# Performance work log

Measured on AMD Instinct MI355X. Metric: run time of the kernel, lower is better.

## Reference

```python
import jax, jax.numpy as jnp
import numpy as np

VOCAB = 50257
EMBED = 256
UNITS = 1024   # dec_units == attention units == GRU units
ENC_D = 1024   # encoder feature dim
B = 64
T_ENC = 128


def setup_inputs() -> dict:
    key = jax.random.key(0)
    ks = jax.random.split(key, 16)
    s = lambda k, *sh: jax.random.normal(k, sh, dtype=jnp.float32) * 0.02
    gru_in = ENC_D + EMBED  # concat(context, embedding)
    return {
        "x": jax.random.randint(ks[0], (B, 1), 0, VOCAB),
        "hidden": jax.random.normal(ks[1], (B, UNITS), dtype=jnp.float32),
        "enc_output": jax.random.normal(ks[2], (B, T_ENC, ENC_D), dtype=jnp.float32),
        "emb": s(ks[3], VOCAB, EMBED),
        "W1": s(ks[4], UNITS, UNITS), "b1": jnp.zeros((UNITS,), jnp.float32),
        "W2": s(ks[5], ENC_D, UNITS), "b2": jnp.zeros((UNITS,), jnp.float32),
        "V": s(ks[6], UNITS, 1), "bV": jnp.zeros((1,), jnp.float32),
        "gru_kernel": s(ks[7], gru_in, 3 * UNITS),
        "gru_rkernel": s(ks[8], UNITS, 3 * UNITS),
        "gru_bias": jnp.zeros((2, 3 * UNITS), jnp.float32),  # reset_after=True: [input_bias, recurrent_bias]
        "fcW": s(ks[9], UNITS, VOCAB), "fcb": jnp.zeros((VOCAB,), jnp.float32),
    }


def reference(x, hidden, enc_output, emb, W1, b1, W2, b2, V, bV,
              gru_kernel, gru_rkernel, gru_bias, fcW, fcb):
    # --- Bahdanau attention ---
    q = hidden[:, None, :] @ W1 + b1                    # [B,1,U]
    k = enc_output @ W2 + b2                            # [B,T,U]
    score = jnp.tanh(q + k) @ V + bV                    # [B,T,1]
    attw = jax.nn.softmax(score, axis=1)                # [B,T,1]
    context = jnp.sum(attw * enc_output, axis=1)        # [B,ENC_D]

    # --- embed token and concat (single time step) ---
    e = emb[x[:, 0]]                                    # [B,EMBED]
    xin = jnp.concatenate([context, e], axis=-1)        # [B,ENC_D+EMBED]

    # --- single GRU step (keras default reset_after=True), initial state zeros
    # (original code calls self.gru(x) without initial_state) ---
    h0 = jnp.zeros((xin.shape[0], UNITS), xin.dtype)
    xz, xr, xh = jnp.split(xin @ gru_kernel + gru_bias[0], 3, axis=-1)
    rz, rr, rh = jnp.split(h0 @ gru_rkernel + gru_bias[1], 3, axis=-1)
    z = jax.nn.sigmoid(xz + rz)
    r = jax.nn.sigmoid(xr + rr)
    hh = jnp.tanh(xh + r * rh)
    h = z * h0 + (1.0 - z) * hh                          # [B,U]

    logits = h @ fcW + fcb                               # [B,VOCAB]
    return logits, h, attw
```

## Files before the change

kernel.cpp:

```cpp
#include <hip/hip_runtime.h>
#include <hip/hip_bf16.h>

#define UNITS 1024
#define EMBED 256
#define TENC  128
#define BATCH 64
#define VOCAB 50257
#define GRU_IN 1280
#define MROWS 8192
#define NCB   8

typedef __bf16 bf16x8 __attribute__((ext_vector_type(8)));
typedef __bf16 bf16x2 __attribute__((ext_vector_type(2)));
typedef float  f32x4  __attribute__((ext_vector_type(4)));
typedef float  f32x4u __attribute__((ext_vector_type(4), aligned(4)));

__global__ __launch_bounds__(256) void gemm_splitk(
    const float* __restrict__ A, const float* __restrict__ B,
    float* __restrict__ Cpart, int M, int N, int K, int Kc)
{
  const int row0  = blockIdx.x * 64;
  const int col0  = blockIdx.y * 64;
  const int kbase = blockIdx.z * Kc;
  const int tid  = threadIdx.x;
  const int lane = tid & 63;
  const int wid  = tid >> 6;
  const int wm   = (wid >> 1) * 32;
  const int wn   = (wid & 1) * 32;

  __shared__ __bf16 As[4][64][8];
  __shared__ __bf16 Bs[4][64][8];

  f32x4 acc[2][2] = {};

  const int ar  = tid >> 2;
  const int akc = (tid & 3) * 8;
  const int bkk = tid >> 4;
  const int bn  = (tid & 15) * 4;

  f32x4 pa0 = {}, pa1 = {}, pb0 = {}, pb1 = {};

  auto LOAD = [&](int k0) {
    if (row0 + ar < M) {
      const float* ap = A + (size_t)(row0 + ar) * K + k0 + akc;
      pa0 = *reinterpret_cast<const f32x4*>(ap);
      pa1 = *reinterpret_cast<const f32x4*>(ap + 4);
    }
    const float* bp0 = B + (size_t)(k0 + bkk) * N + col0 + bn;
    pb0 = *reinterpret_cast<const f32x4*>(bp0);
    pb1 = *reinterpret_cast<const f32x4*>(bp0 + (size_t)16 * N);
  };

  LOAD(kbase);
  const int nt = Kc >> 5;
  for (int t = 0; t < nt; ++t) {
    __syncthreads();
    {
      bf16x8 v;
#pragma unroll
      for (int j = 0; j < 4; ++j) { v[j] = (__bf16)pa0[j]; v[4 + j] = (__bf16)pa1[j]; }
      *reinterpret_cast<bf16x8*>(&As[tid & 3][ar][0]) = v;
#pragma unroll
      for (int j = 0; j < 4; ++j) {
        Bs[bkk >> 3][bn + j][bkk & 7]               = (__bf16)pb0[j];
        Bs[(bkk + 16) >> 3][bn + j][(bkk + 16) & 7] = (__bf16)pb1[j];
      }
    }
    __syncthreads();
    if (t + 1 < nt) LOAD(kbase + ((t + 1) << 5));

    bf16x8 af[2], bfr[2];
#pragma unroll
    for (int f = 0; f < 2; ++f) {
      af[f]  = *reinterpret_cast<const bf16x8*>(&As[lane >> 4][wm + f * 16 + (lane & 15)][0]);
      bfr[f] = *reinterpret_cast<const bf16x8*>(&Bs[lane >> 4][wn + f * 16 + (lane & 15)][0]);
    }
#pragma unroll
    for (int fm = 0; fm < 2; ++fm)
#pragma unroll
      for (int fn = 0; fn < 2; ++fn)
        acc[fm][fn] = __builtin_amdgcn_mfma_f32_16x16x32_bf16(af[fm], bfr[fn], acc[fm][fn], 0, 0, 0);
  }

  float* Cz = Cpart + (size_t)blockIdx.z * M * N;
#pragma unroll
  for (int fm = 0; fm < 2; ++fm) {
    const int rbase = row0 + wm + fm * 16 + (lane >> 4) * 4;
#pragma unroll
    for (int fn = 0; fn < 2; ++fn) {
      const int gc = col0 + wn + fn * 16 + (lane & 15);
#pragma unroll
      for (int r = 0; r < 4; ++r) {
        const int gr = rbase + r;
        if (gr < M) Cz[(size_t)gr * N + gc] = acc[fm][fn][r];
      }
    }
  }
}

__global__ __launch_bounds__(256) void gemm_fc(
    const float* __restrict__ A, const float* __restrict__ B,
    const float* __restrict__ bias, float* __restrict__ C, int N)
{
  const int col0 = blockIdx.x * 64;
  const int tid  = threadIdx.x;
  const int lane = tid & 63;
  const int wid  = tid >> 6;
  const int wm   = (wid >> 1) * 32;
  const int wn   = (wid & 1) * 32;

  __shared__ __bf16 As[4][64][8];
  __shared__ __bf16 Bs[4][64][8];

  f32x4 acc[2][2] = {};

  const int ar  = tid >> 2;
  const int akc = (tid & 3) * 8;
  const int bkk = tid >> 4;
  const int bn  = (tid & 15) * 4;

  f32x4 pa0, pa1, pb0, pb1;

  auto LOAD = [&](int k0) {
    const float* ap = A + (size_t)ar * UNITS + k0 + akc;
    pa0 = *reinterpret_cast<const f32x4*>(ap);
    pa1 = *reinterpret_cast<const f32x4*>(ap + 4);
    const int gn = col0 + bn;
    const float* bp0 = B + (size_t)(k0 + bkk) * N + gn;
    const float* bp1 = bp0 + (size_t)16 * N;
    if (gn + 3 < N) {
      pb0 = __builtin_nontemporal_load(reinterpret_cast<const f32x4u*>(bp0));
      pb1 = __builtin_nontemporal_load(reinterpret_cast<const f32x4u*>(bp1));
    } else {
      pb0 = (f32x4){0,0,0,0}; pb1 = (f32x4){0,0,0,0};
#pragma unroll
      for (int j = 0; j < 4; ++j)
        if (gn + j < N) { pb0[j] = bp0[j]; pb1[j] = bp1[j]; }
    }
  };

  LOAD(0);
  for (int t = 0; t < 32; ++t) {
    __syncthreads();
    {
      bf16x8 v;
#pragma unroll
      for (int j = 0; j < 4; ++j) { v[j] = (__bf16)pa0[j]; v[4 + j] = (__bf16)pa1[j]; }
      *reinterpret_cast<bf16x8*>(&As[tid & 3][ar][0]) = v;
#pragma unroll
      for (int j = 0; j < 4; ++j) {
        Bs[bkk >> 3][bn + j][bkk & 7]               = (__bf16)pb0[j];
        Bs[(bkk + 16) >> 3][bn + j][(bkk + 16) & 7] = (__bf16)pb1[j];
      }
    }
    __syncthreads();
    if (t + 1 < 32) LOAD((t + 1) << 5);

    bf16x8 af[2], bfr[2];
#pragma unroll
    for (int f = 0; f < 2; ++f) {
      af[f]  = *reinterpret_cast<const bf16x8*>(&As[lane >> 4][wm + f * 16 + (lane & 15)][0]);
      bfr[f] = *reinterpret_cast<const bf16x8*>(&Bs[lane >> 4][wn + f * 16 + (lane & 15)][0]);
    }
#pragma unroll
    for (int fm = 0; fm < 2; ++fm)
#pragma unroll
      for (int fn = 0; fn < 2; ++fn)
        acc[fm][fn] = __builtin_amdgcn_mfma_f32_16x16x32_bf16(af[fm], bfr[fn], acc[fm][fn], 0, 0, 0);
  }

#pragma unroll
  for (int fm = 0; fm < 2; ++fm) {
    const int rbase = wm + fm * 16 + (lane >> 4) * 4;
#pragma unroll
    for (int fn = 0; fn < 2; ++fn) {
      const int gc = col0 + wn + fn * 16 + (lane & 15);
      if (gc >= N) continue;
      const float bv = bias[gc];
#pragma unroll
      for (int r = 0; r < 4; ++r)
        __builtin_nontemporal_store(acc[fm][fn][r] + bv, &C[(size_t)(rbase + r) * N + gc]);
    }
  }
}

__global__ __launch_bounds__(256) void gemm_k_score(
    const float* __restrict__ enc, const float* __restrict__ W2,
    const float* __restrict__ b1, const float* __restrict__ b2,
    const float* __restrict__ qpart, const float* __restrict__ Vw,
    float* __restrict__ partial)
{
  const int b    = blockIdx.x;
  const int row0 = b * TENC;
  const int col0 = blockIdx.y * 128;
  const int tid  = threadIdx.x;
  const int lane = tid & 63;
  const int wid  = tid >> 6;
  const int wm   = (wid >> 1) * 64;
  const int wn   = (wid & 1) * 64;

  __shared__ __bf16 As[4][128][8];
  __shared__ __bf16 Bs[4][128][8];
  __shared__ float  sred[2][128];

  f32x4 acc[4][4] = {};

  const int ar  = tid >> 1;
  const int ak  = (tid & 1) * 16;
  const int kkp = (tid >> 4) * 2;
  const int c0  = (tid & 15) * 8;

  f32x4 pa[4], pb[4];

  auto LOAD = [&](int k0) {
    const float* ap = enc + (size_t)(row0 + ar) * UNITS + k0 + ak;
    pa[0] = *reinterpret_cast<const f32x4*>(ap);
    pa[1] = *reinterpret_cast<const f32x4*>(ap + 4);
    pa[2] = *reinterpret_cast<const f32x4*>(ap + 8);
    pa[3] = *reinterpret_cast<const f32x4*>(ap + 12);
    const float* bp0 = W2 + (size_t)(k0 + kkp) * UNITS + col0 + c0;
    pb[0] = *reinterpret_cast<const f32x4*>(bp0);
    pb[1] = *reinterpret_cast<const f32x4*>(bp0 + 4);
    pb[2] = *reinterpret_cast<const f32x4*>(bp0 + UNITS);
    pb[3] = *reinterpret_cast<const f32x4*>(bp0 + UNITS + 4);
  };

  LOAD(0);
  for (int t = 0; t < 32; ++t) {
    __syncthreads();
    {
      bf16x8 v0, v1;
#pragma unroll
      for (int j = 0; j < 4; ++j) {
        v0[j] = (__bf16)pa[0][j]; v0[4 + j] = (__bf16)pa[1][j];
        v1[j] = (__bf16)pa[2][j]; v1[4 + j] = (__bf16)pa[3][j];
      }
      *reinterpret_cast<bf16x8*>(&As[(ak >> 3) + 0][ar][0]) = v0;
      *reinterpret_cast<bf16x8*>(&As[(ak >> 3) + 1][ar][0]) = v1;
      const int bch = kkp >> 3, bk = kkp & 7;
#pragma unroll
      for (int j = 0; j < 8; ++j) {
        const float lo = (j < 4) ? pb[0][j] : pb[1][j - 4];
        const float hi = (j < 4) ? pb[2][j] : pb[3][j - 4];
        bf16x2 pr = { (__bf16)lo, (__bf16)hi };
        *reinterpret_cast<bf16x2*>(&Bs[bch][c0 + j][bk]) = pr;
      }
    }
    __syncthreads();
    if (t + 1 < 32) LOAD((t + 1) << 5);

    bf16x8 af[4], bfr[4];
#pragma unroll
    for (int f = 0; f < 4; ++f) {
      af[f]  = *reinterpret_cast<const bf16x8*>(&As[lane >> 4][wm + f * 16 + (lane & 15)][0]);
      bfr[f] = *reinterpret_cast<const bf16x8*>(&Bs[lane >> 4][wn + f * 16 + (lane & 15)][0]);
    }
#pragma unroll
    for (int fm = 0; fm < 4; ++fm)
#pragma unroll
      for (int fn = 0; fn < 4; ++fn)
        acc[fm][fn] = __builtin_amdgcn_mfma_f32_16x16x32_bf16(af[fm], bfr[fn], acc[fm][fn], 0, 0, 0);
  }

  float rowsum[4][4] = {};
#pragma unroll
  for (int fn = 0; fn < 4; ++fn) {
    const int gc = col0 + wn + fn * 16 + (lane & 15);
    float qv = b1[gc] + b2[gc];
#pragma unroll
    for (int s = 0; s < 4; ++s) qv += qpart[(size_t)s * BATCH * UNITS + (size_t)b * UNITS + gc];
    const float vv = Vw[gc];
#pragma unroll
    for (int fm = 0; fm < 4; ++fm)
#pragma unroll
      for (int r = 0; r < 4; ++r)
        rowsum[fm][r] += tanhf(qv + acc[fm][fn][r]) * vv;
  }
#pragma unroll
  for (int off = 8; off; off >>= 1)
#pragma unroll
    for (int fm = 0; fm < 4; ++fm)
#pragma unroll
      for (int r = 0; r < 4; ++r)
        rowsum[fm][r] += __shfl_xor(rowsum[fm][r], off);
  if ((lane & 15) == 0) {
#pragma unroll
    for (int fm = 0; fm < 4; ++fm)
#pragma unroll
      for (int r = 0; r < 4; ++r)
        sred[wid & 1][wm + fm * 16 + (lane >> 4) * 4 + r] = rowsum[fm][r];
  }
  __syncthreads();
  if (tid < TENC)
    partial[(size_t)blockIdx.y * MROWS + row0 + tid] = sred[0][tid] + sred[1][tid];
}

__global__ __launch_bounds__(256) void ctx_kernel(
    const float* __restrict__ enc, const float* __restrict__ partial,
    const float* __restrict__ bV, const float* __restrict__ emb,
    const int* __restrict__ x, float* __restrict__ attw,
    float* __restrict__ xin)
{
  const int b   = blockIdx.x;
  const int tid = threadIdx.x;
  __shared__ float scs[TENC];
  __shared__ float red[4];

  if (tid < TENC) {
    float s = bV[0];
#pragma unroll
    for (int cb = 0; cb < NCB; ++cb) s += partial[(size_t)cb * MROWS + b * TENC + tid];
    float m = s;
#pragma unroll
    for (int off = 32; off; off >>= 1) m = fmaxf(m, __shfl_xor(m, off));
    if ((tid & 63) == 0) red[tid >> 6] = m;
    scs[tid] = s;
  }
  __syncthreads();
  const float mm = fmaxf(red[0], red[1]);
  if (tid < TENC) {
    const float e = expf(scs[tid] - mm);
    scs[tid] = e;
    float su = e;
#pragma unroll
    for (int off = 32; off; off >>= 1) su += __shfl_xor(su, off);
    if ((tid & 63) == 0) red[2 + (tid >> 6)] = su;
  }
  __syncthreads();
  const float inv = 1.f / (red[2] + red[3]);
  if (tid < TENC) scs[tid] *= inv;
  __syncthreads();

  if (blockIdx.y == 0 && tid < TENC) attw[(size_t)b * TENC + tid] = scs[tid];

  const int n = blockIdx.y * 256 + tid;
  const float* ep = enc + (size_t)b * TENC * UNITS + n;
  float c = 0.f;
#pragma unroll 8
  for (int t = 0; t < TENC; ++t) c += scs[t] * ep[(size_t)t * UNITS];
  xin[(size_t)b * GRU_IN + n] = c;
  if (blockIdx.y == 0)
    xin[(size_t)b * GRU_IN + UNITS + tid] = emb[(size_t)x[b] * EMBED + tid];
}

__global__ __launch_bounds__(256) void gru_pw(
    const float* __restrict__ gpart, const float* __restrict__ gb0,
    const float* __restrict__ gb1, float* __restrict__ h)
{
  const int i = blockIdx.x * 256 + threadIdx.x;
  const int b = i >> 10, n = i & 1023;
  float xz = gb0[n], xr = gb0[1024 + n], xh = gb0[2048 + n];
#pragma unroll
  for (int s = 0; s < 4; ++s) {
    const float* g = gpart + (size_t)s * BATCH * 3072 + (size_t)b * 3072;
    xz += g[n]; xr += g[1024 + n]; xh += g[2048 + n];
  }
  const float rz = gb1[n], rr = gb1[1024 + n], rh = gb1[2048 + n];
  const float z = 1.f / (1.f + expf(-(xz + rz)));
  const float r = 1.f / (1.f + expf(-(xr + rr)));
  const float hh = tanhf(xh + r * rh);
  h[i] = (1.f - z) * hh;
}

extern "C" void kernel_launch(void* const* d_in, const int* in_sizes, int n_in,
                              void* d_out, int out_size, void* d_ws, size_t ws_size,
                              hipStream_t stream)
{
  (void)in_sizes; (void)n_in; (void)out_size; (void)ws_size;
  const int*   x      = (const int*)  d_in[0];
  const float* hidden = (const float*)d_in[1];
  const float* enc    = (const float*)d_in[2];
  const float* emb    = (const float*)d_in[3];
  const float* W1     = (const float*)d_in[4];
  const float* b1     = (const float*)d_in[5];
  const float* W2     = (const float*)d_in[6];
  const float* b2     = (const float*)d_in[7];
  const float* Vw     = (const float*)d_in[8];
  const float* bV     = (const float*)d_in[9];
  const float* gk     = (const float*)d_in[10];
  const float* gb     = (const float*)d_in[12];
  const float* fcW    = (const float*)d_in[13];
  const float* fcb    = (const float*)d_in[14];

  float* ws      = (float*)d_ws;
  float* qpart   = ws;
  float* partial = qpart + 262144;
  float* xin     = partial + 65536;
  float* gpart   = xin + 81920;

  float* out    = (float*)d_out;
  float* logits = out;
  float* hout   = out + (size_t)BATCH * VOCAB;
  float* attw   = hout + BATCH * UNITS;

  hipLaunchKernelGGL(gemm_splitk, dim3(1, 16, 4), dim3(256), 0, stream,
                     hidden, W1, qpart, 64, 1024, 1024, 256);
  hipLaunchKernelGGL(gemm_k_score, dim3(64, NCB), dim3(256), 0, stream,
                     enc, W2, b1, b2, qpart, Vw, partial);
  hipLaunchKernelGGL(ctx_kernel, dim3(64, 4), dim3(256), 0, stream,
                     enc, partial, bV, emb, x, attw, xin);
  hipLaunchKernelGGL(gemm_splitk, dim3(1, 48, 4), dim3(256), 0, stream,
                     xin, gk, gpart, 64, 3072, 1280, 320);
  hipLaunchKernelGGL(gru_pw, dim3(256), dim3(256), 0, stream,
                     gpart, gb, gb + 3072, hout);
  hipLaunchKernelGGL(gemm_fc, dim3((VOCAB + 63) / 64), dim3(256), 0, stream,
                     hout, fcW, fcb, logits, VOCAB);
}
```

Measured before the change: 162.7 us.

## Double-buffer LDS in split-K and FC GEMMs, double split-K factor

```diff
diff --git a/kernel.cpp b/kernel.cpp
--- a/kernel.cpp
+++ b/kernel.cpp
@@ -9,6 +9,7 @@
 #define GRU_IN 1280
 #define MROWS 8192
 #define NCB   8
+#define NSPLIT 8
 
 typedef __bf16 bf16x8 __attribute__((ext_vector_type(8)));
 typedef __bf16 bf16x2 __attribute__((ext_vector_type(2)));
@@ -19,7 +20,6 @@
     const float* __restrict__ A, const float* __restrict__ B,
     float* __restrict__ Cpart, int M, int N, int K, int Kc)
 {
-  const int row0  = blockIdx.x * 64;
   const int col0  = blockIdx.y * 64;
   const int kbase = blockIdx.z * Kc;
   const int tid  = threadIdx.x;
@@ -28,8 +28,8 @@
   const int wm   = (wid >> 1) * 32;
   const int wn   = (wid & 1) * 32;
 
-  __shared__ __bf16 As[4][64][8];
-  __shared__ __bf16 Bs[4][64][8];
+  __shared__ __bf16 As[2][4][64][8];
+  __shared__ __bf16 Bs[2][4][64][8];
 
   f32x4 acc[2][2] = {};
 
@@ -38,62 +38,69 @@
   const int bkk = tid >> 4;
   const int bn  = (tid & 15) * 4;
 
-  f32x4 pa0 = {}, pa1 = {}, pb0 = {}, pb1 = {};
-
-  auto LOAD = [&](int k0) {
-    if (row0 + ar < M) {
-      const float* ap = A + (size_t)(row0 + ar) * K + k0 + akc;
-      pa0 = *reinterpret_cast<const f32x4*>(ap);
-      pa1 = *reinterpret_cast<const f32x4*>(ap + 4);
-    }
+  f32x4 pa0[2], pa1[2], pb0[2], pb1[2];
+
+  auto LOAD = [&](int k0, int s) {
+    const float* ap = A + (size_t)ar * K + k0 + akc;
+    pa0[s] = *reinterpret_cast<const f32x4*>(ap);
+    pa1[s] = *reinterpret_cast<const f32x4*>(ap + 4);
     const float* bp0 = B + (size_t)(k0 + bkk) * N + col0 + bn;
-    pb0 = *reinterpret_cast<const f32x4*>(bp0);
-    pb1 = *reinterpret_cast<const f32x4*>(bp0 + (size_t)16 * N);
-  };
-
-  LOAD(kbase);
-  const int nt = Kc >> 5;
-  for (int t = 0; t < nt; ++t) {
-    __syncthreads();
-    {
-      bf16x8 v;
-#pragma unroll
-      for (int j = 0; j < 4; ++j) { v[j] = (__bf16)pa0[j]; v[4 + j] = (__bf16)pa1[j]; }
-      *reinterpret_cast<bf16x8*>(&As[tid & 3][ar][0]) = v;
-#pragma unroll
-      for (int j = 0; j < 4; ++j) {
-        Bs[bkk >> 3][bn + j][bkk & 7]               = (__bf16)pb0[j];
-        Bs[(bkk + 16) >> 3][bn + j][(bkk + 16) & 7] = (__bf16)pb1[j];
-      }
-    }
-    __syncthreads();
-    if (t + 1 < nt) LOAD(kbase + ((t + 1) << 5));
-
+    pb0[s] = *reinterpret_cast<const f32x4*>(bp0);
+    pb1[s] = *reinterpret_cast<const f32x4*>(bp0 + (size_t)16 * N);
+  };
+  auto STAGE = [&](int s, int bb) {
+    bf16x8 v;
+#pragma unroll
+    for (int j = 0; j < 4; ++j) { v[j] = (__bf16)pa0[s][j]; v[4 + j] = (__bf16)pa1[s][j]; }
+    *reinterpret_cast<bf16x8*>(&As[bb][tid & 3][ar][0]) = v;
+#pragma unroll
+    for (int j = 0; j < 4; ++j) {
+      Bs[bb][bkk >> 3][bn + j][bkk & 7]               = (__bf16)pb0[s][j];
+      Bs[bb][(bkk + 16) >> 3][bn + j][(bkk + 16) & 7] = (__bf16)pb1[s][j];
+    }
+  };
+  auto COMPUTE = [&](int bb) {
     bf16x8 af[2], bfr[2];
 #pragma unroll
     for (int f = 0; f < 2; ++f) {
-      af[f]  = *reinterpret_cast<const bf16x8*>(&As[lane >> 4][wm + f * 16 + (lane & 15)][0]);
-      bfr[f] = *reinterpret_cast<const bf16x8*>(&Bs[lane >> 4][wn + f * 16 + (lane & 15)][0]);
+      af[f]  = *reinterpret_cast<const bf16x8*>(&As[bb][lane >> 4][wm + f * 16 + (lane & 15)][0]);
+      bfr[f] = *reinterpret_cast<const bf16x8*>(&Bs[bb][lane >> 4][wn + f * 16 + (lane & 15)][0]);
     }
 #pragma unroll
     for (int fm = 0; fm < 2; ++fm)
 #pragma unroll
       for (int fn = 0; fn < 2; ++fn)
         acc[fm][fn] = __builtin_amdgcn_mfma_f32_16x16x32_bf16(af[fm], bfr[fn], acc[fm][fn], 0, 0, 0);
+  };
+
+  const int nt = Kc >> 5;
+  LOAD(kbase, 0);
+  LOAD(kbase + 32, 1);
+  STAGE(0, 0);
+  __syncthreads();
+  for (int t = 0; t < nt; t += 2) {
+    if (t + 2 < nt) LOAD(kbase + ((t + 2) << 5), 0);
+    COMPUTE(0);
+    if (t + 1 < nt) STAGE(1, 1);
+    __syncthreads();
+    if (t + 1 < nt) {
+      if (t + 3 < nt) LOAD(kbase + ((t + 3) << 5), 1);
+      COMPUTE(1);
+      if (t + 2 < nt) STAGE(0, 0);
+      __syncthreads();
+    }
   }
 
   float* Cz = Cpart + (size_t)blockIdx.z * M * N;
 #pragma unroll
   for (int fm = 0; fm < 2; ++fm) {
-    const int rbase = row0 + wm + fm * 16 + (lane >> 4) * 4;
+    const int rbase = wm + fm * 16 + (lane >> 4) * 4;
 #pragma unroll
     for (int fn = 0; fn < 2; ++fn) {
       const int gc = col0 + wn + fn * 16 + (lane & 15);
 #pragma unroll
-      for (int r = 0; r < 4; ++r) {
-        const int gr = rbase + r;
-        if (gr < M) Cz[(size_t)gr * N + gc] = acc[fm][fn][r];
-      }
+      for (int r = 0; r < 4; ++r)
+        Cz[(size_t)(rbase + r) * N + gc] = acc[fm][fn][r];
     }
   }
 }
@@ -109,8 +116,8 @@
   const int wm   = (wid >> 1) * 32;
   const int wn   = (wid & 1) * 32;
 
-  __shared__ __bf16 As[4][64][8];
-  __shared__ __bf16 Bs[4][64][8];
+  __shared__ __bf16 As[2][4][64][8];
+  __shared__ __bf16 Bs[2][4][64][8];
 
   f32x4 acc[2][2] = {};
 
@@ -118,55 +125,67 @@
   const int akc = (tid & 3) * 8;
   const int bkk = tid >> 4;
   const int bn  = (tid & 15) * 4;
-
-  f32x4 pa0, pa1, pb0, pb1;
-
-  auto LOAD = [&](int k0) {
+  const int gn  = col0 + bn;
+  const bool okb = (gn + 3 < N);
+
+  f32x4 pa0[2], pa1[2], pb0[2], pb1[2];
+
+  auto LOAD = [&](int k0, int s) {
     const float* ap = A + (size_t)ar * UNITS + k0 + akc;
-    pa0 = *reinterpret_cast<const f32x4*>(ap);
-    pa1 = *reinterpret_cast<const f32x4*>(ap + 4);
-    const int gn = col0 + bn;
+    pa0[s] = *reinterpret_cast<const f32x4*>(ap);
+    pa1[s] = *reinterpret_cast<const f32x4*>(ap + 4);
     const float* bp0 = B + (size_t)(k0 + bkk) * N + gn;
     const float* bp1 = bp0 + (size_t)16 * N;
-    if (gn + 3 < N) {
-      pb0 = __builtin_nontemporal_load(reinterpret_cast<const f32x4u*>(bp0));
-      pb1 = __builtin_nontemporal_load(reinterpret_cast<const f32x4u*>(bp1));
+    if (okb) {
+      pb0[s] = *reinterpret_cast<const f32x4u*>(bp0);
+      pb1[s] = *reinterpret_cast<const f32x4u*>(bp1);
     } else {
-      pb0 = (f32x4){0,0,0,0}; pb1 = (f32x4){0,0,0,0};
+      f32x4 t0 = {0,0,0,0}, t1 = {0,0,0,0};
 #pragma unroll
       for (int j = 0; j < 4; ++j)
-        if (gn + j < N) { pb0[j] = bp0[j]; pb1[j] = bp1[j]; }
-    }
-  };
-
-  LOAD(0);
-  for (int t = 0; t < 32; ++t) {
-    __syncthreads();
-    {
-      bf16x8 v;
-#pragma unroll
-      for (int j = 0; j < 4; ++j) { v[j] = (__bf16)pa0[j]; v[4 + j] = (__bf16)pa1[j]; }
-      *reinterpret_cast<bf16x8*>(&As[tid & 3][ar][0]) = v;
-#pragma unroll
-      for (int j = 0; j < 4; ++j) {
-        Bs[bkk >> 3][bn + j][bkk & 7]               = (__bf16)pb0[j];
-        Bs[(bkk + 16) >> 3][bn + j][(bkk + 16) & 7] = (__bf16)pb1[j];
-      }
-    }
-    __syncthreads();
-    if (t + 1 < 32) LOAD((t + 1) << 5);
-
+        if (gn + j < N) { t0[j] = bp0[j]; t1[j] = bp1[j]; }
+      pb0[s] = t0; pb1[s] = t1;
+    }
+  };
+  auto STAGE = [&](int s, int bb) {
+    bf16x8 v;
+#pragma unroll
+    for (int j = 0; j < 4; ++j) { v[j] = (__bf16)pa0[s][j]; v[4 + j] = (__bf16)pa1[s][j]; }
+    *reinterpret_cast<bf16x8*>(&As[bb][tid & 3][ar][0]) = v;
+#pragma unroll
+    for (int j = 0; j < 4; ++j) {
+      Bs[bb][bkk >> 3][bn + j][bkk & 7]               = (__bf16)pb0[s][j];
+      Bs[bb][(bkk + 16) >> 3][bn + j][(bkk + 16) & 7] = (__bf16)pb1[s][j];
+    }
+  };
+  auto COMPUTE = [&](int bb) {
     bf16x8 af[2], bfr[2];
 #pragma unroll
     for (int f = 0; f < 2; ++f) {
-      af[f]  = *reinterpret_cast<const bf16x8*>(&As[lane >> 4][wm + f * 16 + (lane & 15)][0]);
-      bfr[f] = *reinterpret_cast<const bf16x8*>(&Bs[lane >> 4][wn + f * 16 + (lane & 15)][0]);
+      af[f]  = *reinterpret_cast<const bf16x8*>(&As[bb][lane >> 4][wm + f * 16 + (lane & 15)][0]);
+      bfr[f] = *reinterpret_cast<const bf16x8*>(&Bs[bb][lane >> 4][wn + f * 16 + (lane & 15)][0]);
     }
 #pragma unroll
     for (int fm = 0; fm < 2; ++fm)
 #pragma unroll
       for (int fn = 0; fn < 2; ++fn)
         acc[fm][fn] = __builtin_amdgcn_mfma_f32_16x16x32_bf16(af[fm], bfr[fn], acc[fm][fn], 0, 0, 0);
+  };
+
+  LOAD(0, 0);
+  LOAD(32, 1);
+  STAGE(0, 0);
+  __syncthreads();
+#pragma unroll 1
+  for (int t = 0; t < 32; t += 2) {
+    if (t + 2 < 32) LOAD((t + 2) << 5, 0);
+    COMPUTE(0);
+    STAGE(1, 1);
+    __syncthreads();
+    if (t + 3 < 32) LOAD((t + 3) << 5, 1);
+    COMPUTE(1);
+    if (t + 2 < 32) STAGE(0, 0);
+    __syncthreads();
   }
 
 #pragma unroll
@@ -268,7 +287,8 @@
     const int gc = col0 + wn + fn * 16 + (lane & 15);
     float qv = b1[gc] + b2[gc];
 #pragma unroll
-    for (int s = 0; s < 4; ++s) qv += qpart[(size_t)s * BATCH * UNITS + (size_t)b * UNITS + gc];
+    for (int s = 0; s < NSPLIT; ++s)
+      qv += qpart[(size_t)s * BATCH * UNITS + (size_t)b * UNITS + gc];
     const float vv = Vw[gc];
 #pragma unroll
     for (int fm = 0; fm < 4; ++fm)
@@ -351,7 +371,7 @@
   const int b = i >> 10, n = i & 1023;
   float xz = gb0[n], xr = gb0[1024 + n], xh = gb0[2048 + n];
 #pragma unroll
-  for (int s = 0; s < 4; ++s) {
+  for (int s = 0; s < NSPLIT; ++s) {
     const float* g = gpart + (size_t)s * BATCH * 3072 + (size_t)b * 3072;
     xz += g[n]; xr += g[1024 + n]; xh += g[2048 + n];
   }
@@ -384,7 +404,7 @@
 
   float* ws      = (float*)d_ws;
   float* qpart   = ws;
-  float* partial = qpart + 262144;
+  float* partial = qpart + 524288;
   float* xin     = partial + 65536;
   float* gpart   = xin + 81920;
 
@@ -393,14 +413,14 @@
   float* hout   = out + (size_t)BATCH * VOCAB;
   float* attw   = hout + BATCH * UNITS;
 
-  hipLaunchKernelGGL(gemm_splitk, dim3(1, 16, 4), dim3(256), 0, stream,
-                     hidden, W1, qpart, 64, 1024, 1024, 256);
+  hipLaunchKernelGGL(gemm_splitk, dim3(1, 16, NSPLIT), dim3(256), 0, stream,
+                     hidden, W1, qpart, 64, 1024, 1024, 128);
   hipLaunchKernelGGL(gemm_k_score, dim3(64, NCB), dim3(256), 0, stream,
                      enc, W2, b1, b2, qpart, Vw, partial);
   hipLaunchKernelGGL(ctx_kernel, dim3(64, 4), dim3(256), 0, stream,
                      enc, partial, bV, emb, x, attw, xin);
-  hipLaunchKernelGGL(gemm_splitk, dim3(1, 48, 4), dim3(256), 0, stream,
-                     xin, gk, gpart, 64, 3072, 1280, 320);
+  hipLaunchKernelGGL(gemm_splitk, dim3(1, 48, NSPLIT), dim3(256), 0, stream,
+                     xin, gk, gpart, 64, 3072, 1280, 160);
   hipLaunchKernelGGL(gru_pw, dim3(256), dim3(256), 0, stream,
                      gpart, gb, gb + 3072, hout);
   hipLaunchKernelGGL(gemm_fc, dim3((VOCAB + 63) / 64), dim3(256), 0, stream,
```

New measurement: 153.2 us. 1.06x faster.
